# Kernel optimization log

Measured on AMD Instinct MI355X. Metric: run time of the kernel, lower is better.

The kernel has to match this reference:

```python
import jax, jax.numpy as jnp
import numpy as np

B, T, N, D = 8, 12, 883, 128
H, C = 8, 16          # heads, out_channels per head (D = H*C, concat=True)
E = 7000              # edges per graph instance
FF = 2048             # feed_forward_dim
NEG_SLOPE = 0.2       # GATv2Conv default negative_slope


def setup_inputs() -> dict:
    key = jax.random.key(0)
    ks = jax.random.split(key, 16)
    s = 0.05
    return {
        "x": jax.random.normal(ks[0], (B, T, N, D), jnp.float32),
        "edge_index": jax.random.randint(ks[1], (2, E), 0, N, dtype=jnp.int64),
        # GATv2Conv params (lin_l, lin_r each have bias by default; att vector; final bias)
        "Wl": jax.random.normal(ks[2], (D, H * C), jnp.float32) * s,
        "bl": jnp.zeros((H * C,), jnp.float32),
        "Wr": jax.random.normal(ks[3], (D, H * C), jnp.float32) * s,
        "br": jnp.zeros((H * C,), jnp.float32),
        "att": jax.random.normal(ks[4], (H, C), jnp.float32) * s,
        "bias_gat": jnp.zeros((H * C,), jnp.float32),
        # FFN
        "W1": jax.random.normal(ks[5], (D, FF), jnp.float32) * s,
        "b1": jnp.zeros((FF,), jnp.float32),
        "W2": jax.random.normal(ks[6], (FF, D), jnp.float32) * s,
        "b2": jnp.zeros((D,), jnp.float32),
        # LayerNorms
        "g1": jnp.ones((D,), jnp.float32),
        "be1": jnp.zeros((D,), jnp.float32),
        "g2": jnp.ones((D,), jnp.float32),
        "be2": jnp.zeros((D,), jnp.float32),
    }


def _layer_norm(x, g, b, eps=1e-5):
    mu = x.mean(-1, keepdims=True)
    var = ((x - mu) ** 2).mean(-1, keepdims=True)
    return (x - mu) * jax.lax.rsqrt(var + eps) * g + b


def _forward(x, edge_index, Wl, bl, Wr, br, att, bias_gat,
             W1, b1, W2, b2, g1, be1, g2, be2):
    B_, T_, N_, D_ = x.shape
    BT = B_ * T_
    TN = BT * N_
    # expand shared edge_index across B*T instances (per torch code)
    offsets = jnp.arange(BT, dtype=edge_index.dtype) * N_
    ee = (edge_index[None, :, :] + offsets[:, None, None]).transpose(1, 0, 2).reshape(2, -1)
    # PyG GATv2Conv default: add self loops
    loops = jnp.arange(TN, dtype=edge_index.dtype)
    src = jnp.concatenate([ee[0], loops])  # message source j
    dst = jnp.concatenate([ee[1], loops])  # message target i

    xf = x.reshape(TN, D_)
    x_l = (xf @ Wl + bl).reshape(TN, H, C)
    x_r = (xf @ Wr + br).reshape(TN, H, C)

    # GATv2 attention: leaky_relu(x_l[j] + x_r[i]) . att
    e = x_l[src] + x_r[dst]                        # [Etot, H, C]
    e = jnp.where(e > 0, e, NEG_SLOPE * e)
    score = jnp.einsum('ehc,hc->eh', e, att)       # [Etot, H]

    # segment softmax over incoming edges per target node
    smax = jax.ops.segment_max(score, dst, num_segments=TN)
    a = jnp.exp(score - smax[dst])
    denom = jax.ops.segment_sum(a, dst, num_segments=TN)
    alpha = a / denom[dst]                          # [Etot, H]

    # scatter-add aggregation of alpha * x_l[src]
    agg = jax.ops.segment_sum(alpha[:, :, None] * x_l[src], dst, num_segments=TN)
    x_gat = (agg.reshape(TN, H * C) + bias_gat).reshape(B_, T_, N_, D_)

    h = _layer_norm(x + x_gat, g1, be1)
    ff = (jnp.maximum(h.reshape(-1, D_) @ W1 + b1, 0.0) @ W2 + b2).reshape(h.shape)
    return _layer_norm(h + ff, g2, be2)


def reference(x, edge_index, Wl, bl, Wr, br, att, bias_gat,
              W1, b1, W2, b2, g1, be1, g2, be2):
    return _forward(x, edge_index, Wl, bl, Wr, br, att, bias_gat,
                    W1, b1, W2, b2, g1, be1, g2, be2)
```

## Files before the change

### kernel.cpp

```cpp
#include <hip/hip_runtime.h>
#include <stdint.h>

typedef unsigned short u16;

#define TN    84768
#define NNODE 883
#define DD    128
#define EE    7000
#define FFDIM 2048

typedef short bf16x8 __attribute__((ext_vector_type(8)));
typedef float f32x4  __attribute__((ext_vector_type(4)));
typedef __attribute__((address_space(3))) u16 lds_u16;
typedef const __attribute__((address_space(1))) u16 glb_u16;

__device__ __forceinline__ float bf2f(u16 u) {
    unsigned int x = ((unsigned int)u) << 16;
    return __uint_as_float(x);
}
__device__ __forceinline__ u16 f2bf(float f) {
    unsigned int x = __float_as_uint(f);
    x += 0x7FFFu + ((x >> 16) & 1u);
    return (u16)(x >> 16);
}
__device__ __forceinline__ u16 cleanu(u16 u) {
    return (((u >> 7) & 0xFF) == 0xFF) ? (u16)0 : u;
}
__device__ __forceinline__ u16 cleanf(float f) {
    unsigned b = __float_as_uint(f);
    if (((b >> 23) & 0xFF) == 0xFF) return 0;
    return cleanu(f2bf(f));
}
__device__ __forceinline__ float loadx(const void* p, size_t i, int f32) {
    if (f32) {
        float v = ((const float*)p)[i];
        unsigned b = __float_as_uint(v);
        if (((b >> 23) & 0xFF) == 0xFF) v = 0.f;
        return v;
    }
    return bf2f(cleanu(((const u16*)p)[i]));
}

__global__ __launch_bounds__(256) void k_detect(const unsigned* __restrict__ x,
                                                int* __restrict__ flag) {
    __shared__ int cnt;
    if (threadIdx.x == 0) cnt = 0;
    __syncthreads();
    unsigned w = x[threadIdx.x];
    unsigned e = (w >> 7) & 0xFF;
    int ok = (e >= 96 && e <= 144) || ((w & 0xFFFFu) == 0);
    atomicAdd(&cnt, ok);
    __syncthreads();
    if (threadIdx.x == 0) flag[0] = (cnt < 200) ? 1 : 0;
}

__global__ __launch_bounds__(256) void k_prep(const void* Wl, const void* Wr,
                                              const void* W1, const void* W2,
                                              const void* bl, const void* br,
                                              const void* att, const void* bgat,
                                              const void* b1, const void* b2,
                                              const void* g1, const void* be1,
                                              const void* g2, const void* be2,
                                              u16* __restrict__ wlrT,
                                              u16* __restrict__ w1T,
                                              u16* __restrict__ w2T,
                                              u16* __restrict__ canon,
                                              const int* __restrict__ flag) {
    int f32 = *flag;
    int i = blockIdx.x * 256 + threadIdx.x;
    if (i < 16384) {
        int r = i >> 7, c = i & 127;
        u16 v = f32 ? cleanf(((const float*)Wl)[i]) : cleanu(((const u16*)Wl)[i]);
        wlrT[c * 128 + r] = v;
    } else if (i < 32768) {
        int idx = i - 16384;
        int r = idx >> 7, c = idx & 127;
        u16 v = f32 ? cleanf(((const float*)Wr)[idx]) : cleanu(((const u16*)Wr)[idx]);
        wlrT[16384 + c * 128 + r] = v;
    } else if (i < 294912) {
        int idx = i - 32768;
        int r = idx >> 11, c = idx & 2047;
        u16 v = f32 ? cleanf(((const float*)W1)[idx]) : cleanu(((const u16*)W1)[idx]);
        w1T[c * 128 + r] = v;
    } else if (i < 557056) {
        int idx = i - 294912;
        int r = idx >> 7, c = idx & 127;
        u16 v = f32 ? cleanf(((const float*)W2)[idx]) : cleanu(((const u16*)W2)[idx]);
        w2T[c * 2048 + r] = v;
    } else if (i < 560256) {
        int p = i - 557056;
        const void* src; int off;
        if      (p < 128)  { src = bl;   off = 0; }
        else if (p < 256)  { src = br;   off = 128; }
        else if (p < 384)  { src = att;  off = 256; }
        else if (p < 512)  { src = bgat; off = 384; }
        else if (p < 2560) { src = b1;   off = 512; }
        else if (p < 2688) { src = b2;   off = 2560; }
        else if (p < 2816) { src = g1;   off = 2688; }
        else if (p < 2944) { src = be1;  off = 2816; }
        else if (p < 3072) { src = g2;   off = 2944; }
        else               { src = be2;  off = 3072; }
        int j = p - off;
        canon[p] = f32 ? cleanf(((const float*)src)[j]) : cleanu(((const u16*)src)[j]);
    }
}

__global__ __launch_bounds__(1024) void k_csr(const int* __restrict__ ew,
                                              int* __restrict__ row_off,
                                              int* __restrict__ col) {
    __shared__ int cnt[NNODE];
    __shared__ int offs[NNODE + 1];
    __shared__ int cur[NNODE];
    __shared__ int flag;
    int tid = threadIdx.x;
    if (tid == 0) flag = 0;
    for (int i = tid; i < NNODE; i += 1024) cnt[i] = 0;
    __syncthreads();
    int f = 0;
    for (int j = tid; j < EE; j += 1024) f |= ew[2 * j + 1];
    if (f) atomicOr(&flag, 1);
    __syncthreads();
    bool is32 = (flag != 0);
    for (int e = tid; e < EE; e += 1024) {
        int dst = is32 ? ew[EE + e] : ew[2 * EE + 2 * e];
        if ((unsigned)dst < NNODE) atomicAdd(&cnt[dst], 1);
    }
    __syncthreads();
    if (tid == 0) {
        int run = 0;
        for (int i = 0; i < NNODE; ++i) { offs[i] = run; run += cnt[i]; }
        offs[NNODE] = run;
    }
    __syncthreads();
    for (int i = tid; i < NNODE; i += 1024) cur[i] = offs[i];
    __syncthreads();
    for (int e = tid; e < EE; e += 1024) {
        int src = is32 ? ew[e] : ew[2 * e];
        int dst = is32 ? ew[EE + e] : ew[2 * EE + 2 * e];
        if ((unsigned)dst < NNODE && (unsigned)src < NNODE) {
            int p = atomicAdd(&cur[dst], 1);
            if (p < EE) col[p] = src;
        }
    }
    __syncthreads();
    for (int i = tid; i <= NNODE; i += 1024) row_off[i] = offs[i];
}

__global__ __launch_bounds__(256) void k_linlr(const void* __restrict__ xraw,
                                               const u16* __restrict__ wlrT,
                                               const u16* __restrict__ canon,
                                               u16* __restrict__ xl, u16* __restrict__ xr,
                                               const int* __restrict__ flag) {
    __shared__ __align__(16) u16 a_tile[64 * 136];
    int f32 = *flag;
    int tid = threadIdx.x;
    int m0 = blockIdx.x * 64;
    for (int it = 0; it < 4; ++it) {
        int idx = it * 256 + tid;
        int row = idx >> 4, cc = idx & 15;
        int gm = m0 + row;
        u16 tmp[8];
#pragma unroll
        for (int j = 0; j < 8; ++j) tmp[j] = 0;
        if (gm < TN) {
            size_t base = (size_t)gm * DD + cc * 8;
            if (f32) {
                float4 v0 = *(const float4*)((const float*)xraw + base);
                float4 v1 = *(const float4*)((const float*)xraw + base + 4);
                tmp[0] = cleanf(v0.x); tmp[1] = cleanf(v0.y);
                tmp[2] = cleanf(v0.z); tmp[3] = cleanf(v0.w);
                tmp[4] = cleanf(v1.x); tmp[5] = cleanf(v1.y);
                tmp[6] = cleanf(v1.z); tmp[7] = cleanf(v1.w);
            } else {
                uint4 v = *(const uint4*)((const u16*)xraw + base);
                unsigned wv[4] = {v.x, v.y, v.z, v.w};
#pragma unroll
                for (int j = 0; j < 8; ++j)
                    tmp[j] = cleanu((u16)((wv[j >> 1] >> ((j & 1) * 16)) & 0xFFFFu));
            }
        }
        uint4 o;
        o.x = (unsigned)tmp[0] | ((unsigned)tmp[1] << 16);
        o.y = (unsigned)tmp[2] | ((unsigned)tmp[3] << 16);
        o.z = (unsigned)tmp[4] | ((unsigned)tmp[5] << 16);
        o.w = (unsigned)tmp[6] | ((unsigned)tmp[7] << 16);
        *(uint4*)(a_tile + row * 136 + cc * 8) = o;
    }
    __syncthreads();
    int wave = tid >> 6, lane = tid & 63, n16 = lane & 15, q = lane >> 4;
    f32x4 acc[16];
#pragma unroll
    for (int t = 0; t < 16; ++t) acc[t] = (f32x4){0, 0, 0, 0};
    const u16* arow = a_tile + (16 * wave + n16) * 136;
#pragma unroll
    for (int ks = 0; ks < 4; ++ks) {
        bf16x8 a = *(const bf16x8*)(arow + ks * 32 + q * 8);
#pragma unroll
        for (int t = 0; t < 16; ++t) {
            bf16x8 b = *(const bf16x8*)(wlrT + ((size_t)(t * 16 + n16)) * DD + ks * 32 + q * 8);
            acc[t] = __builtin_amdgcn_mfma_f32_16x16x32_bf16(a, b, acc[t], 0, 0, 0);
        }
    }
#pragma unroll
    for (int t = 0; t < 16; ++t) {
        int cc = (t & 7) * 16 + n16;
        float bias = bf2f(canon[(t < 8 ? 0 : 128) + cc]);
        u16* dst = (t < 8 ? xl : xr);
#pragma unroll
        for (int reg = 0; reg < 4; ++reg) {
            int mrow = m0 + 16 * wave + 4 * q + reg;
            if (mrow < TN) dst[(size_t)mrow * DD + cc] = f2bf(acc[t][reg] + bias);
        }
    }
}

__device__ __forceinline__ float segsum16(float p) {
    p += __shfl_xor(p, 1, 16);
    p += __shfl_xor(p, 2, 16);
    p += __shfl_xor(p, 4, 16);
    p += __shfl_xor(p, 8, 16);
    return p;
}

__global__ __launch_bounds__(256) void k_gat(const void* __restrict__ xraw,
                                             const u16* __restrict__ xl,
                                             const u16* xr,
                                             const u16* __restrict__ canon,
                                             const int* __restrict__ row_off,
                                             const int* __restrict__ col,
                                             u16* h1,
                                             const int* __restrict__ flag) {
    int f32 = *flag;
    int tid = threadIdx.x;
    int wave = tid >> 6, lane = tid & 63;
    int g = blockIdx.x * 4 + wave;
    int bt = g / NNODE;
    int i = g - bt * NNODE;
    size_t gbase = (size_t)g * DD;
    const u16* xlrow0 = xl + (size_t)bt * NNODE * DD;
    int c2 = lane * 2;
    unsigned uxr = *(const unsigned*)(xr + gbase + c2);
    float xr0 = __uint_as_float(uxr << 16);
    float xr1 = __uint_as_float(uxr & 0xFFFF0000u);
    unsigned uat = *(const unsigned*)(canon + 256 + c2);
    float at0 = __uint_as_float(uat << 16);
    float at1 = __uint_as_float(uat & 0xFFFF0000u);
    unsigned uxs = *(const unsigned*)(xl + gbase + c2);
    float xs0 = __uint_as_float(uxs << 16);
    float xs1 = __uint_as_float(uxs & 0xFFFF0000u);
    float t0 = xs0 + xr0, t1 = xs1 + xr1;
    t0 = fmaxf(t0, 0.2f * t0); t1 = fmaxf(t1, 0.2f * t1);
    float p = t0 * at0 + t1 * at1;
    p += __shfl_xor(p, 1, 8);
    p += __shfl_xor(p, 2, 8);
    p += __shfl_xor(p, 4, 8);
    p = fminf(fmaxf(p, -30.f), 30.f);
    float w = __expf(p);
    float denom = w;
    float a0 = w * xs0, a1 = w * xs1;
    int r0 = row_off[i], r1 = row_off[i + 1];
    for (int e = r0; e < r1; ++e) {
        int j = __builtin_amdgcn_readfirstlane(col[e]);
        if ((unsigned)j >= NNODE) continue;
        unsigned uj = *(const unsigned*)(xlrow0 + (size_t)j * DD + c2);
        float x0 = __uint_as_float(uj << 16);
        float x1 = __uint_as_float(uj & 0xFFFF0000u);
        float u0 = x0 + xr0, u1 = x1 + xr1;
        u0 = fmaxf(u0, 0.2f * u0); u1 = fmaxf(u1, 0.2f * u1);
        float q = u0 * at0 + u1 * at1;
        q += __shfl_xor(q, 1, 8);
        q += __shfl_xor(q, 2, 8);
        q += __shfl_xor(q, 4, 8);
        q = fminf(fmaxf(q, -30.f), 30.f);
        float ww = __expf(q);
        denom += ww;
        a0 += ww * x0;
        a1 += ww * x1;
    }
    float inv = 1.f / denom;
    unsigned ubg = *(const unsigned*)(canon + 384 + c2);
    float res0, res1;
    if (f32) {
        float2 rr = *(const float2*)((const float*)xraw + gbase + c2);
        unsigned b0 = __float_as_uint(rr.x), b1 = __float_as_uint(rr.y);
        res0 = (((b0 >> 23) & 0xFF) == 0xFF) ? 0.f : rr.x;
        res1 = (((b1 >> 23) & 0xFF) == 0xFF) ? 0.f : rr.y;
    } else {
        unsigned ux = *(const unsigned*)((const u16*)xraw + gbase + c2);
        res0 = bf2f(cleanu((u16)(ux & 0xFFFFu)));
        res1 = bf2f(cleanu((u16)(ux >> 16)));
    }
    float pre0 = a0 * inv + __uint_as_float(ubg << 16) + res0;
    float pre1 = a1 * inv + __uint_as_float(ubg & 0xFFFF0000u) + res1;
    float sum = pre0 + pre1, sq = pre0 * pre0 + pre1 * pre1;
    for (int off = 32; off; off >>= 1) {
        sum += __shfl_xor(sum, off);
        sq  += __shfl_xor(sq, off);
    }
    float mu = sum * (1.0f / 128.0f);
    float var = fmaxf(sq * (1.0f / 128.0f) - mu * mu, 0.f);
    float rs = rsqrtf(var + 1e-5f);
    unsigned ug = *(const unsigned*)(canon + 2688 + c2);
    unsigned ub = *(const unsigned*)(canon + 2816 + c2);
    float h0 = (pre0 - mu) * rs * __uint_as_float(ug << 16) + __uint_as_float(ub << 16);
    float h1v = (pre1 - mu) * rs * __uint_as_float(ug & 0xFFFF0000u) + __uint_as_float(ub & 0xFFFF0000u);
    unsigned out = (unsigned)f2bf(h0) | ((unsigned)f2bf(h1v) << 16);
    *(unsigned*)(h1 + gbase + c2) = out;
}

__global__ __launch_bounds__(256, 3) void k_ffn(const u16* __restrict__ h1,
                                                const u16* __restrict__ w1T,
                                                const u16* __restrict__ w2T,
                                                const u16* __restrict__ canon,
                                                void* __restrict__ outraw,
                                                const int* __restrict__ flag) {
    __shared__ __align__(16) u16 w1b[64 * 128];
    __shared__ __align__(16) u16 w2b[128 * 64];
    __shared__ __align__(16) u16 s_t[64 * 72];
    int f32 = *flag;
    int tid = threadIdx.x;
    int wave = tid >> 6, lane = tid & 63, n16 = lane & 15, q = lane >> 4;
    int m0 = blockIdx.x * 64;
    int swz = n16 & 7;
    bf16x8 af[4];
    {
        int gm = m0 + 16 * wave + n16;
#pragma unroll
        for (int ks = 0; ks < 4; ++ks) {
            if (gm < TN) {
                uint4 v = *(const uint4*)(h1 + (size_t)gm * DD + ks * 32 + q * 8);
                af[ks] = *(const bf16x8*)&v;
            } else {
                uint4 z = make_uint4(0, 0, 0, 0);
                af[ks] = *(const bf16x8*)&z;
            }
        }
    }
    f32x4 acc2[8];
#pragma unroll
    for (int t = 0; t < 8; ++t) acc2[t] = (f32x4){0, 0, 0, 0};
    int w1r[4], w1b_log[4];
#pragma unroll
    for (int i = 0; i < 4; ++i) {
        w1r[i] = 16 * wave + 4 * i + (lane >> 4);
        w1b_log[i] = (lane & 15) ^ (w1r[i] & 7);
    }
    int w2r[4], w2b_log[4];
#pragma unroll
    for (int i = 0; i < 4; ++i) {
        w2r[i] = 32 * wave + 8 * i + (lane >> 3);
        w2b_log[i] = (lane & 7) ^ (w2r[i] & 7);
    }
    const u16* srow_r = s_t + (16 * wave + n16) * 72;
    u16* srow_w = s_t + (16 * wave + 4 * q) * 72;
    for (int ch = 0; ch < 32; ++ch) {
        int f0 = ch * 64;
        __syncthreads();
#pragma unroll
        for (int i = 0; i < 4; ++i) {
            glb_u16* g1 = (glb_u16*)(w1T + (size_t)(f0 + w1r[i]) * DD + w1b_log[i] * 8);
            lds_u16* l1 = (lds_u16*)(w1b + (16 * wave + 4 * i) * 128);
            __builtin_amdgcn_global_load_lds((const __attribute__((address_space(1))) unsigned*)g1,
                                             (__attribute__((address_space(3))) unsigned*)l1,
                                             16, 0, 0);
        }
#pragma unroll
        for (int i = 0; i < 4; ++i) {
            glb_u16* g2 = (glb_u16*)(w2T + (size_t)w2r[i] * FFDIM + f0 + w2b_log[i] * 8);
            lds_u16* l2 = (lds_u16*)(w2b + (32 * wave + 8 * i) * 64);
            __builtin_amdgcn_global_load_lds((const __attribute__((address_space(1))) unsigned*)g2,
                                             (__attribute__((address_space(3))) unsigned*)l2,
                                             16, 0, 0);
        }
        __syncthreads();
#pragma unroll
        for (int t = 0; t < 4; ++t) {
            f32x4 a1 = (f32x4){0, 0, 0, 0};
#pragma unroll
            for (int ks = 0; ks < 4; ++ks) {
                bf16x8 b = *(const bf16x8*)(w1b + (t * 16 + n16) * 128 + (((ks * 4 + q) ^ swz) * 8));
                a1 = __builtin_amdgcn_mfma_f32_16x16x32_bf16(af[ks], b, a1, 0, 0, 0);
            }
            float bb = bf2f(canon[512 + f0 + t * 16 + n16]);
#pragma unroll
            for (int reg = 0; reg < 4; ++reg) {
                float v = a1[reg] + bb;
                v = v > 0.f ? v : 0.f;
                srow_w[reg * 72 + t * 16 + n16] = f2bf(v);
            }
        }
        asm volatile("" ::: "memory");
#pragma unroll
        for (int ks2 = 0; ks2 < 2; ++ks2) {
            bf16x8 a2 = *(const bf16x8*)(srow_r + ks2 * 32 + q * 8);
#pragma unroll
            for (int t = 0; t < 8; ++t) {
                bf16x8 b = *(const bf16x8*)(w2b + (t * 16 + n16) * 64 + (((ks2 * 4 + q) ^ swz) * 8));
                acc2[t] = __builtin_amdgcn_mfma_f32_16x16x32_bf16(a2, b, acc2[t], 0, 0, 0);
            }
        }
        asm volatile("" ::: "memory");
    }
    float b2v[8], g2v[8], e2v[8];
#pragma unroll
    for (int t = 0; t < 8; ++t) {
        int col = t * 16 + n16;
        b2v[t] = bf2f(canon[2560 + col]);
        g2v[t] = bf2f(canon[2944 + col]);
        e2v[t] = bf2f(canon[3072 + col]);
    }
#pragma unroll
    for (int reg = 0; reg < 4; ++reg) {
        int row = 16 * wave + 4 * q + reg;
        int gm = m0 + row;
        bool ok = gm < TN;
        size_t gb = (size_t)(ok ? gm : 0) * DD;
        float v[8]; float s1 = 0.f, s2 = 0.f;
#pragma unroll
        for (int t = 0; t < 8; ++t) {
            float hres = bf2f(h1[gb + t * 16 + n16]);
            v[t] = acc2[t][reg] + b2v[t] + hres;
            s1 += v[t]; s2 += v[t] * v[t];
        }
        s1 = segsum16(s1);
        s2 = segsum16(s2);
        float mu = s1 * (1.f / 128.f);
        float var = fmaxf(s2 * (1.f / 128.f) - mu * mu, 0.f);
        float rs = rsqrtf(var + 1e-5f);
        if (ok) {
#pragma unroll
            for (int t = 0; t < 8; ++t) {
                float r = (v[t] - mu) * rs * g2v[t] + e2v[t];
                if (f32) ((float*)outraw)[gb + t * 16 + n16] = r;
                else     ((u16*)outraw)[gb + t * 16 + n16] = f2bf(r);
            }
        }
    }
}

extern "C" void kernel_launch(void* const* d_in, const int* in_sizes, int n_in,
                              void* d_out, int out_size, void* d_ws, size_t ws_size,
                              hipStream_t stream) {
    const void* x    = d_in[0];
    const int* eidx  = (const int*)d_in[1];
    const void* Wl   = d_in[2];
    const void* bl   = d_in[3];
    const void* Wr   = d_in[4];
    const void* br   = d_in[5];
    const void* att  = d_in[6];
    const void* bgat = d_in[7];
    const void* W1   = d_in[8];
    const void* b1   = d_in[9];
    const void* W2   = d_in[10];
    const void* b2   = d_in[11];
    const void* g1   = d_in[12];
    const void* be1  = d_in[13];
    const void* g2   = d_in[14];
    const void* be2  = d_in[15];

    char* ws = (char*)d_ws;
    int* flag   = (int*)(ws);
    int* rowoff = (int*)(ws + 4096);
    int* colw   = (int*)(ws + 8192);
    u16* canon  = (u16*)(ws + 36864);
    u16* wlrT   = (u16*)(ws + 65536);
    u16* w1T    = (u16*)(ws + 131072);
    u16* w2T    = (u16*)(ws + 655360);
    u16* xl     = (u16*)(ws + 1179648);
    u16* xr     = (u16*)(ws + 22880256);
    u16* h1     = xr;

    k_csr<<<1, 1024, 0, stream>>>(eidx, rowoff, colw);
    k_detect<<<1, 256, 0, stream>>>((const unsigned*)x, flag);
    k_prep<<<2189, 256, 0, stream>>>(Wl, Wr, W1, W2, bl, br, att, bgat, b1, b2,
                                     g1, be1, g2, be2, wlrT, w1T, w2T, canon, flag);
    k_linlr<<<(TN + 63) / 64, 256, 0, stream>>>(x, wlrT, canon, xl, xr, flag);
    k_gat<<<TN / 4, 256, 0, stream>>>(x, xl, xr, canon, rowoff, colw, h1, flag);
    k_ffn<<<(TN + 63) / 64, 256, 0, stream>>>(h1, w1T, w2T, canon, d_out, flag);
}
```

Measured before the change: 439.0 us.

## Double FFN row tile per block to reuse staged weights across two subtiles

The fused FFN kernel now processes 128 rows per block instead of 64, with each wave computing two 16-row subtiles that share every B-fragment loaded from the LDS weight chunks. This halves the number of W1/W2 chunk loads and barriers per row and issues more MFMAs per LDS read. The cost is doubled accumulator registers (acc2 grows to 64 floats) plus a larger LDS intermediate buffer, which may lower occupancy under the existing launch bound of 3 blocks and leaves half as many blocks in the grid. An unused helper function is also removed.

```diff
diff --git a/kernel.cpp b/kernel.cpp
--- a/kernel.cpp
+++ b/kernel.cpp
@@ -30,15 +30,6 @@
     unsigned b = __float_as_uint(f);
     if (((b >> 23) & 0xFF) == 0xFF) return 0;
     return cleanu(f2bf(f));
-}
-__device__ __forceinline__ float loadx(const void* p, size_t i, int f32) {
-    if (f32) {
-        float v = ((const float*)p)[i];
-        unsigned b = __float_as_uint(v);
-        if (((b >> 23) & 0xFF) == 0xFF) v = 0.f;
-        return v;
-    }
-    return bf2f(cleanu(((const u16*)p)[i]));
 }
 
 __global__ __launch_bounds__(256) void k_detect(const unsigned* __restrict__ x,
@@ -316,29 +307,32 @@
                                                 const int* __restrict__ flag) {
     __shared__ __align__(16) u16 w1b[64 * 128];
     __shared__ __align__(16) u16 w2b[128 * 64];
-    __shared__ __align__(16) u16 s_t[64 * 72];
+    __shared__ __align__(16) u16 s_t[128 * 72];
     int f32 = *flag;
     int tid = threadIdx.x;
     int wave = tid >> 6, lane = tid & 63, n16 = lane & 15, q = lane >> 4;
-    int m0 = blockIdx.x * 64;
+    int m0 = blockIdx.x * 128;
     int swz = n16 & 7;
-    bf16x8 af[4];
-    {
-        int gm = m0 + 16 * wave + n16;
+    bf16x8 af[2][4];
+#pragma unroll
+    for (int sub = 0; sub < 2; ++sub) {
+        int gm = m0 + 32 * wave + 16 * sub + n16;
 #pragma unroll
         for (int ks = 0; ks < 4; ++ks) {
             if (gm < TN) {
                 uint4 v = *(const uint4*)(h1 + (size_t)gm * DD + ks * 32 + q * 8);
-                af[ks] = *(const bf16x8*)&v;
+                af[sub][ks] = *(const bf16x8*)&v;
             } else {
                 uint4 z = make_uint4(0, 0, 0, 0);
-                af[ks] = *(const bf16x8*)&z;
-            }
-        }
-    }
-    f32x4 acc2[8];
-#pragma unroll
-    for (int t = 0; t < 8; ++t) acc2[t] = (f32x4){0, 0, 0, 0};
+                af[sub][ks] = *(const bf16x8*)&z;
+            }
+        }
+    }
+    f32x4 acc2[2][8];
+#pragma unroll
+    for (int sub = 0; sub < 2; ++sub)
+#pragma unroll
+        for (int t = 0; t < 8; ++t) acc2[sub][t] = (f32x4){0, 0, 0, 0};
     int w1r[4], w1b_log[4];
 #pragma unroll
     for (int i = 0; i < 4; ++i) {
@@ -351,8 +345,10 @@
         w2r[i] = 32 * wave + 8 * i + (lane >> 3);
         w2b_log[i] = (lane & 7) ^ (w2r[i] & 7);
     }
-    const u16* srow_r = s_t + (16 * wave + n16) * 72;
-    u16* srow_w = s_t + (16 * wave + 4 * q) * 72;
+    u16* srow_w0 = s_t + (32 * wave + 4 * q) * 72;
+    u16* srow_w1 = s_t + (32 * wave + 16 + 4 * q) * 72;
+    const u16* srow_r0 = s_t + (32 * wave + n16) * 72;
+    const u16* srow_r1 = s_t + (32 * wave + 16 + n16) * 72;
     for (int ch = 0; ch < 32; ++ch) {
         int f0 = ch * 64;
         __syncthreads();
@@ -375,28 +371,35 @@
         __syncthreads();
 #pragma unroll
         for (int t = 0; t < 4; ++t) {
-            f32x4 a1 = (f32x4){0, 0, 0, 0};
+            f32x4 a10 = (f32x4){0, 0, 0, 0};
+            f32x4 a11 = (f32x4){0, 0, 0, 0};
 #pragma unroll
             for (int ks = 0; ks < 4; ++ks) {
                 bf16x8 b = *(const bf16x8*)(w1b + (t * 16 + n16) * 128 + (((ks * 4 + q) ^ swz) * 8));
-                a1 = __builtin_amdgcn_mfma_f32_16x16x32_bf16(af[ks], b, a1, 0, 0, 0);
+                a10 = __builtin_amdgcn_mfma_f32_16x16x32_bf16(af[0][ks], b, a10, 0, 0, 0);
+                a11 = __builtin_amdgcn_mfma_f32_16x16x32_bf16(af[1][ks], b, a11, 0, 0, 0);
             }
             float bb = bf2f(canon[512 + f0 + t * 16 + n16]);
 #pragma unroll
             for (int reg = 0; reg < 4; ++reg) {
-                float v = a1[reg] + bb;
-                v = v > 0.f ? v : 0.f;
-                srow_w[reg * 72 + t * 16 + n16] = f2bf(v);
+                float v0 = a10[reg] + bb;
+                float v1 = a11[reg] + bb;
+                v0 = v0 > 0.f ? v0 : 0.f;
+                v1 = v1 > 0.f ? v1 : 0.f;
+                srow_w0[reg * 72 + t * 16 + n16] = f2bf(v0);
+                srow_w1[reg * 72 + t * 16 + n16] = f2bf(v1);
             }
         }
         asm volatile("" ::: "memory");
 #pragma unroll
         for (int ks2 = 0; ks2 < 2; ++ks2) {
-            bf16x8 a2 = *(const bf16x8*)(srow_r + ks2 * 32 + q * 8);
+            bf16x8 a20 = *(const bf16x8*)(srow_r0 + ks2 * 32 + q * 8);
+            bf16x8 a21 = *(const bf16x8*)(srow_r1 + ks2 * 32 + q * 8);
 #pragma unroll
             for (int t = 0; t < 8; ++t) {
                 bf16x8 b = *(const bf16x8*)(w2b + (t * 16 + n16) * 64 + (((ks2 * 4 + q) ^ swz) * 8));
-                acc2[t] = __builtin_amdgcn_mfma_f32_16x16x32_bf16(a2, b, acc2[t], 0, 0, 0);
+                acc2[0][t] = __builtin_amdgcn_mfma_f32_16x16x32_bf16(a20, b, acc2[0][t], 0, 0, 0);
+                acc2[1][t] = __builtin_amdgcn_mfma_f32_16x16x32_bf16(a21, b, acc2[1][t], 0, 0, 0);
             }
         }
         asm volatile("" ::: "memory");
@@ -410,29 +413,32 @@
         e2v[t] = bf2f(canon[3072 + col]);
     }
 #pragma unroll
-    for (int reg = 0; reg < 4; ++reg) {
-        int row = 16 * wave + 4 * q + reg;
-        int gm = m0 + row;
-        bool ok = gm < TN;
-        size_t gb = (size_t)(ok ? gm : 0) * DD;
-        float v[8]; float s1 = 0.f, s2 = 0.f;
-#pragma unroll
-        for (int t = 0; t < 8; ++t) {
-            float hres = bf2f(h1[gb + t * 16 + n16]);
-            v[t] = acc2[t][reg] + b2v[t] + hres;
-            s1 += v[t]; s2 += v[t] * v[t];
-        }
-        s1 = segsum16(s1);
-        s2 = segsum16(s2);
-        float mu = s1 * (1.f / 128.f);
-        float var = fmaxf(s2 * (1.f / 128.f) - mu * mu, 0.f);
-        float rs = rsqrtf(var + 1e-5f);
-        if (ok) {
+    for (int sub = 0; sub < 2; ++sub) {
+#pragma unroll
+        for (int reg = 0; reg < 4; ++reg) {
+            int row = 32 * wave + 16 * sub + 4 * q + reg;
+            int gm = m0 + row;
+            bool ok = gm < TN;
+            size_t gb = (size_t)(ok ? gm : 0) * DD;
+            float v[8]; float s1 = 0.f, s2 = 0.f;
 #pragma unroll
             for (int t = 0; t < 8; ++t) {
-                float r = (v[t] - mu) * rs * g2v[t] + e2v[t];
-                if (f32) ((float*)outraw)[gb + t * 16 + n16] = r;
-                else     ((u16*)outraw)[gb + t * 16 + n16] = f2bf(r);
+                float hres = bf2f(h1[gb + t * 16 + n16]);
+                v[t] = acc2[sub][t][reg] + b2v[t] + hres;
+                s1 += v[t]; s2 += v[t] * v[t];
+            }
+            s1 = segsum16(s1);
+            s2 = segsum16(s2);
+            float mu = s1 * (1.f / 128.f);
+            float var = fmaxf(s2 * (1.f / 128.f) - mu * mu, 0.f);
+            float rs = rsqrtf(var + 1e-5f);
+            if (ok) {
+#pragma unroll
+                for (int t = 0; t < 8; ++t) {
+                    float r = (v[t] - mu) * rs * g2v[t] + e2v[t];
+                    if (f32) ((float*)outraw)[gb + t * 16 + n16] = r;
+                    else     ((u16*)outraw)[gb + t * 16 + n16] = f2bf(r);
+                }
             }
         }
     }
@@ -476,5 +482,5 @@
                                      g1, be1, g2, be2, wlrT, w1T, w2T, canon, flag);
     k_linlr<<<(TN + 63) / 64, 256, 0, stream>>>(x, wlrT, canon, xl, xr, flag);
     k_gat<<<TN / 4, 256, 0, stream>>>(x, xl, xr, canon, rowoff, colw, h1, flag);
-    k_ffn<<<(TN + 63) / 64, 256, 0, stream>>>(h1, w1T, w2T, canon, d_out, flag);
-}
+    k_ffn<<<(TN + 127) / 128, 256, 0, stream>>>(h1, w1T, w2T, canon, d_out, flag);
+}
```

New measurement: 400.0 us. 1.1x faster.
